# Performance work log

Hardware: AMD Instinct MI355X
Metric: run time of the kernel (lower is better)

## Reference

```python
import jax, jax.numpy as jnp
import numpy as np

B, T, D = 4, 2048, 1024
H = 16
HD = D // H  # 64


def setup_inputs() -> dict:
    key = jax.random.key(0)
    ks = jax.random.split(key, 5)
    scale = 0.02
    x = jax.random.normal(ks[0], (B, T, D), dtype=jnp.float32)
    W_qkv = jax.random.normal(ks[1], (D, 3 * D), dtype=jnp.float32) * scale
    b_qkv = jnp.zeros((3 * D,), dtype=jnp.float32)
    W_proj = jax.random.normal(ks[2], (D, D), dtype=jnp.float32) * scale
    b_proj = jnp.zeros((D,), dtype=jnp.float32)
    return {"x": x, "W_qkv": W_qkv, "b_qkv": b_qkv, "W_proj": W_proj, "b_proj": b_proj}


def reference(x, W_qkv, b_qkv, W_proj, b_proj):
    b, t, c = x.shape
    qkv = x @ W_qkv + b_qkv  # [b, t, 3c]
    q, k, v = jnp.split(qkv, 3, axis=-1)
    # [b, h, t, hd]
    q = q.reshape(b, t, H, HD).transpose(0, 2, 1, 3)
    k = k.reshape(b, t, H, HD).transpose(0, 2, 1, 3)
    v = v.reshape(b, t, H, HD).transpose(0, 2, 1, 3)
    att = jnp.einsum('bhqd,bhkd->bhqk', q, k) / jnp.sqrt(jnp.float32(HD))
    causal = jnp.tril(jnp.ones((t, t), dtype=bool))
    att = jnp.where(causal[None, None], att, jnp.float32(-jnp.inf))
    att = jax.nn.softmax(att, axis=-1)
    y = jnp.einsum('bhqk,bhkd->bhqd', att, v)
    y = y.transpose(0, 2, 1, 3).reshape(b, t, c)
    return y @ W_proj + b_proj
```

## Files before the change

kernel.cpp:

```cpp
#include <hip/hip_runtime.h>
#include <hip/hip_bf16.h>
#include <cmath>
#include <cstdint>

#define B_ 4
#define T_ 2048
#define D_ 1024
#define H_ 16
#define HD_ 64
#define M_ (B_*T_)
#define NQKV_ 3072

#define SCALE_Q 0.18033688011112042f

typedef float f32x4 __attribute__((ext_vector_type(4)));
typedef float f32x16 __attribute__((ext_vector_type(16)));
typedef __bf16 bf16x8 __attribute__((ext_vector_type(8)));
typedef __bf16 bf16x4 __attribute__((ext_vector_type(4)));

#define MFMA16(a, b, c) __builtin_amdgcn_mfma_f32_16x16x32_bf16((a), (b), (c), 0, 0, 0)
#define MFMA32(a, b, c) __builtin_amdgcn_mfma_f32_32x32x16_bf16((a), (b), (c), 0, 0, 0)

#if defined(__has_builtin)
#if __has_builtin(__builtin_amdgcn_global_load_lds)
#define HAVE_GLDS 1
#endif
#if __has_builtin(__builtin_amdgcn_permlane32_swap)
#define HAVE_PLSWAP 1
#endif
#endif

#ifdef HAVE_GLDS
#define GLDS16(g, l) __builtin_amdgcn_global_load_lds( \
    (const __attribute__((address_space(1))) void*)(g), \
    (__attribute__((address_space(3))) void*)(l), 16, 0, 0)
#endif

__device__ inline float hexp2(float x) {
  float r; asm("v_exp_f32 %0, %1" : "=v"(r) : "v"(x)); return r;
}

__device__ inline uint32_t pack2bf(float a, float b) {
  union { __bf16 h[2]; uint32_t u; } x;
  x.h[0] = (__bf16)a; x.h[1] = (__bf16)b;
  return x.u;
}

__global__ __launch_bounds__(256) void k_cvt_bf16(const float4* __restrict__ in,
                                                  bf16x4* __restrict__ out, int n4) {
  int i = blockIdx.x * 256 + threadIdx.x;
  if (i >= n4) return;
  float4 v = in[i];
  bf16x4 o;
  o[0] = (__bf16)v.x; o[1] = (__bf16)v.y; o[2] = (__bf16)v.z; o[3] = (__bf16)v.w;
  out[i] = o;
}

__global__ __launch_bounds__(256) void k_transpose_cvt(const float* __restrict__ in,
                                                       __bf16* __restrict__ out,
                                                       int R, int C) {
  __shared__ float tile[64][65];
  int r0 = blockIdx.y * 64, c0 = blockIdx.x * 64;
#pragma unroll
  for (int i = 0; i < 16; ++i) {
    int e = threadIdx.x + i * 256;
    int lr = e >> 6, lc = e & 63;
    tile[lr][lc] = in[(size_t)(r0 + lr) * C + c0 + lc];
  }
  __syncthreads();
#pragma unroll
  for (int i = 0; i < 16; ++i) {
    int e = threadIdx.x + i * 256;
    int lc = e >> 6, lr = e & 63;
    out[(size_t)(c0 + lc) * R + r0 + lr] = (__bf16)tile[lr][lc];
  }
}

__global__ __launch_bounds__(256) void k_gemm_qkv(const __bf16* __restrict__ A,
                                                  const __bf16* __restrict__ Bt,
                                                  const float* __restrict__ bias,
                                                  __bf16* __restrict__ Qb,
                                                  __bf16* __restrict__ Kb,
                                                  __bf16* __restrict__ Vt) {
  __shared__ __bf16 lA[128 * 64];
  __shared__ __bf16 lB[192 * 64];
  const int tid = threadIdx.x;
  const int lane = tid & 63, w = tid >> 6;
  const int wr = w >> 1, wc = w & 1;
  const int r15 = lane & 15, rg = lane >> 4;
  const int mb = blockIdx.y, nb = blockIdx.x;
  const int K = D_;
  const int nt = K >> 6;

  const f32x4 zero = {0.f, 0.f, 0.f, 0.f};
  f32x4 acc[4][6];
#pragma unroll
  for (int m = 0; m < 4; ++m)
#pragma unroll
    for (int n = 0; n < 6; ++n) acc[m][n] = zero;

  const __bf16* Ab = A + (size_t)(mb * 128) * K;
  const __bf16* Bb = Bt + (size_t)(nb * 192) * K;

  for (int t = 0; t < nt; ++t) {
    __syncthreads();
#pragma unroll
    for (int i = 0; i < 4; ++i) {
      const int c = tid + i * 256;
      const int rA = c >> 3, g = (c & 7) ^ (rA & 7);
#ifdef HAVE_GLDS
      GLDS16(Ab + (size_t)rA * K + t * 64 + g * 8, &lA[c * 8]);
#else
      bf16x8 v = *(const bf16x8*)(Ab + (size_t)rA * K + t * 64 + g * 8);
      *(bf16x8*)(&lA[c * 8]) = v;
#endif
    }
#pragma unroll
    for (int i = 0; i < 6; ++i) {
      const int c = tid + i * 256;
      const int rB = c >> 3, g = (c & 7) ^ (rB & 7);
#ifdef HAVE_GLDS
      GLDS16(Bb + (size_t)rB * K + t * 64 + g * 8, &lB[c * 8]);
#else
      bf16x8 v = *(const bf16x8*)(Bb + (size_t)rB * K + t * 64 + g * 8);
      *(bf16x8*)(&lB[c * 8]) = v;
#endif
    }
    __syncthreads();
#pragma unroll
    for (int ksub = 0; ksub < 2; ++ksub) {
      const int cc = (ksub * 4 + rg) ^ (r15 & 7);
      bf16x8 af[4];
#pragma unroll
      for (int m = 0; m < 4; ++m) {
        const int row = wr * 64 + m * 16 + r15;
        af[m] = *(const bf16x8*)(&lA[(row * 8 + cc) * 8]);
      }
#pragma unroll
      for (int n = 0; n < 6; ++n) {
        const int row = wc * 96 + n * 16 + r15;
        bf16x8 bfr = *(const bf16x8*)(&lB[(row * 8 + cc) * 8]);
#pragma unroll
        for (int m = 0; m < 4; ++m)
          acc[m][n] = MFMA16(af[m], bfr, acc[m][n]);
      }
    }
  }

  const int row0 = mb * 128 + wr * 64;
  const int col0 = nb * 192 + wc * 96;
#pragma unroll
  for (int m = 0; m < 4; ++m) {
#pragma unroll
    for (int n = 0; n < 6; ++n) {
      const int c = col0 + n * 16 + r15;
      const int r0 = row0 + m * 16 + rg * 4;
      const int which = c >> 10, cc = c & 1023;
      const int b = r0 >> 11, t0 = r0 & 2047;
      float v[4];
#pragma unroll
      for (int j = 0; j < 4; ++j) v[j] = acc[m][n][j] + bias[c];
      if (which == 0) {
        int hh = cc >> 6, hd = cc & 63;
#pragma unroll
        for (int j = 0; j < 4; ++j)
          Qb[((size_t)(b * H_ + hh) * T_ + t0 + j) * HD_ + hd] = (__bf16)(v[j] * SCALE_Q);
      } else if (which == 1) {
        int hh = cc >> 6, hd = cc & 63;
#pragma unroll
        for (int j = 0; j < 4; ++j)
          Kb[((size_t)(b * H_ + hh) * T_ + t0 + j) * HD_ + hd] = (__bf16)v[j];
      } else {
        int hh = cc >> 6, hd = cc & 63;
        bf16x4 pk;
#pragma unroll
        for (int j = 0; j < 4; ++j) pk[j] = (__bf16)v[j];
        *(bf16x4*)(Vt + ((size_t)(b * H_ + hh) * HD_ + hd) * T_ + t0) = pk;
      }
    }
  }
}

__global__ __launch_bounds__(256) void k_gemm_proj(const __bf16* __restrict__ A,
                                                   const __bf16* __restrict__ Bt,
                                                   const float* __restrict__ bias,
                                                   float* __restrict__ Cf,
                                                   int K, int N) {
  __shared__ __bf16 lA[128 * 64];
  __shared__ __bf16 lB[128 * 64];
  const int tid = threadIdx.x;
  const int lane = tid & 63, w = tid >> 6;
  const int wr = w >> 1, wc = w & 1;
  const int r15 = lane & 15, rg = lane >> 4;
  const int mb = blockIdx.y, nb = blockIdx.x;
  const int nt = K >> 6;

  const f32x4 zero = {0.f, 0.f, 0.f, 0.f};
  f32x4 acc[4][4];
#pragma unroll
  for (int m = 0; m < 4; ++m)
#pragma unroll
    for (int n = 0; n < 4; ++n) acc[m][n] = zero;

  const __bf16* Ab = A + (size_t)(mb * 128) * K;
  const __bf16* Bb = Bt + (size_t)(nb * 128) * K;

  for (int t = 0; t < nt; ++t) {
    __syncthreads();
#pragma unroll
    for (int i = 0; i < 4; ++i) {
      const int c = tid + i * 256;
      const int rA = c >> 3, g = (c & 7) ^ (rA & 7);
#ifdef HAVE_GLDS
      GLDS16(Ab + (size_t)rA * K + t * 64 + g * 8, &lA[c * 8]);
#else
      bf16x8 v = *(const bf16x8*)(Ab + (size_t)rA * K + t * 64 + g * 8);
      *(bf16x8*)(&lA[c * 8]) = v;
#endif
    }
#pragma unroll
    for (int i = 0; i < 4; ++i) {
      const int c = tid + i * 256;
      const int rB = c >> 3, g = (c & 7) ^ (rB & 7);
#ifdef HAVE_GLDS
      GLDS16(Bb + (size_t)rB * K + t * 64 + g * 8, &lB[c * 8]);
#else
      bf16x8 v = *(const bf16x8*)(Bb + (size_t)rB * K + t * 64 + g * 8);
      *(bf16x8*)(&lB[c * 8]) = v;
#endif
    }
    __syncthreads();
#pragma unroll
    for (int ksub = 0; ksub < 2; ++ksub) {
      bf16x8 af[4], bfr[4];
#pragma unroll
      for (int m = 0; m < 4; ++m) {
        const int row = wr * 64 + m * 16 + r15;
        const int cc = (ksub * 4 + rg) ^ (r15 & 7);
        af[m] = *(const bf16x8*)(&lA[(row * 8 + cc) * 8]);
      }
#pragma unroll
      for (int n = 0; n < 4; ++n) {
        const int row = wc * 64 + n * 16 + r15;
        const int cc = (ksub * 4 + rg) ^ (r15 & 7);
        bfr[n] = *(const bf16x8*)(&lB[(row * 8 + cc) * 8]);
      }
#pragma unroll
      for (int m = 0; m < 4; ++m)
#pragma unroll
        for (int n = 0; n < 4; ++n)
          acc[m][n] = MFMA16(af[m], bfr[n], acc[m][n]);
    }
  }

  const int row0 = mb * 128 + wr * 64;
  const int col0 = nb * 128 + wc * 64;
#pragma unroll
  for (int m = 0; m < 4; ++m)
#pragma unroll
    for (int n = 0; n < 4; ++n)
#pragma unroll
      for (int j = 0; j < 4; ++j) {
        int r = row0 + m * 16 + rg * 4 + j;
        int c = col0 + n * 16 + r15;
        Cf[(size_t)r * N + c] = acc[m][n][j] + bias[c];
      }
}

__global__ __launch_bounds__(256) void k_attn(const __bf16* __restrict__ Qb,
                                              const __bf16* __restrict__ Kb,
                                              const __bf16* __restrict__ Vt,
                                              __bf16* __restrict__ Obuf) {
  __shared__ __bf16 lK[2][64 * 64];
  __shared__ __bf16 lV[2][64 * 64];
  const int tid = threadIdx.x;
  const int lane = tid & 63, w = tid >> 6;
  const int l31 = lane & 31, hi = lane >> 5;
  const int bh = blockIdx.x;
  const int b = bh >> 4, h = bh & 15;
  const __bf16* Qh = Qb + (size_t)bh * T_ * HD_;
  const __bf16* Kh = Kb + (size_t)bh * T_ * HD_;
  const __bf16* Vh = Vt + (size_t)bh * HD_ * T_;

  const int sRow0 = tid >> 3, sSw0 = (((tid) & 7) ^ (sRow0 & 7)) * 8;
  const int c1s = tid + 256;
  const int sRow1 = c1s >> 3, sSw1 = ((c1s & 7) ^ (sRow1 & 7)) * 8;

  auto STAGE = [&](int bufi, int kv0) {
#ifdef HAVE_GLDS
    GLDS16(Kh + (size_t)(kv0 + sRow0) * HD_ + sSw0, &lK[bufi][tid * 8]);
    GLDS16(Kh + (size_t)(kv0 + sRow1) * HD_ + sSw1, &lK[bufi][(tid + 256) * 8]);
    GLDS16(Vh + (size_t)sRow0 * T_ + kv0 + sSw0, &lV[bufi][tid * 8]);
    GLDS16(Vh + (size_t)sRow1 * T_ + kv0 + sSw1, &lV[bufi][(tid + 256) * 8]);
#else
    bf16x8 k0 = *(const bf16x8*)(Kh + (size_t)(kv0 + sRow0) * HD_ + sSw0);
    bf16x8 k1 = *(const bf16x8*)(Kh + (size_t)(kv0 + sRow1) * HD_ + sSw1);
    bf16x8 v0 = *(const bf16x8*)(Vh + (size_t)sRow0 * T_ + kv0 + sSw0);
    bf16x8 v1 = *(const bf16x8*)(Vh + (size_t)sRow1 * T_ + kv0 + sSw1);
    *(bf16x8*)(&lK[bufi][tid * 8]) = k0;
    *(bf16x8*)(&lK[bufi][(tid + 256) * 8]) = k1;
    *(bf16x8*)(&lV[bufi][tid * 8]) = v0;
    *(bf16x8*)(&lV[bufi][(tid + 256) * 8]) = v1;
#endif
  };

  int buf = 0;
  STAGE(0, 0);

  auto process_half = [&](int s, int nst, bool hasNext) {
    const int q0w = s * 128 + w * 32;
    bf16x8 qf[4];
#pragma unroll
    for (int ks = 0; ks < 4; ++ks)
      qf[ks] = *(const bf16x8*)(Qh + (size_t)(q0w + l31) * HD_ + ks * 16 + hi * 8);

    f32x16 o0, o1;
#pragma unroll
    for (int i = 0; i < 16; ++i) { o0[i] = 0.f; o1[i] = 0.f; }
    float lpart = 0.f;

    for (int i = 0; i < nst; ++i) {
      const int kv0 = i * 64;
      if (i + 1 < nst) STAGE(buf ^ 1, (i + 1) * 64);
      else if (hasNext) STAGE(buf ^ 1, 0);

      if (kv0 <= q0w + 31) {
        const bool masked = (kv0 + 63) > q0w;
        bf16x8 kf[2][4];
#pragma unroll
        for (int seg = 0; seg < 2; ++seg)
#pragma unroll
          for (int ks = 0; ks < 4; ++ks)
            kf[seg][ks] = *(const bf16x8*)(&lK[buf][(seg * 32 + l31) * 64 +
                                                   (((ks * 2 + hi) ^ (l31 & 7)) * 8)]);
        f32x16 s0, s1;
#pragma unroll
        for (int r = 0; r < 16; ++r) { s0[r] = 0.f; s1[r] = 0.f; }
        __builtin_amdgcn_s_setprio(1);
#pragma unroll
        for (int ks = 0; ks < 4; ++ks) s0 = MFMA32(kf[0][ks], qf[ks], s0);
#pragma unroll
        for (int ks = 0; ks < 4; ++ks) s1 = MFMA32(kf[1][ks], qf[ks], s1);
        __builtin_amdgcn_s_setprio(0);

        if (masked) {
#pragma unroll
          for (int r = 0; r < 16; ++r) {
            int rr = (r & 3) + 8 * (r >> 2) + 4 * hi;
            if (kv0 + rr > q0w + l31) s0[r] = -INFINITY;
            if (kv0 + 32 + rr > q0w + l31) s1[r] = -INFINITY;
          }
        }
        float rs = 0.f;
#pragma unroll
        for (int r = 0; r < 16; ++r) {
          s0[r] = hexp2(s0[r]); s1[r] = hexp2(s1[r]);
          rs += s0[r] + s1[r];
        }
        lpart += rs;

        bf16x8 vf[2][4];
#pragma unroll
        for (int dh = 0; dh < 2; ++dh)
#pragma unroll
          for (int ks = 0; ks < 4; ++ks)
            vf[dh][ks] = *(const bf16x8*)(&lV[buf][(dh * 32 + l31) * 64 +
                                                   (((ks * 2 + hi) ^ (l31 & 7)) * 8)]);

#pragma unroll
        for (int ks = 0; ks < 4; ++ks) {
          const f32x16& sv = (ks < 2) ? s0 : s1;
          const int off = (ks & 1) * 8;
          uint32_t w0 = pack2bf(sv[off + 0], sv[off + 1]);
          uint32_t w1 = pack2bf(sv[off + 2], sv[off + 3]);
          uint32_t w2 = pack2bf(sv[off + 4], sv[off + 5]);
          uint32_t w3 = pack2bf(sv[off + 6], sv[off + 7]);
          union { uint32_t u[4]; bf16x8 v; } pa;
#ifdef HAVE_PLSWAP
          auto rA = __builtin_amdgcn_permlane32_swap((int)w0, (int)w2, false, false);
          auto rB = __builtin_amdgcn_permlane32_swap((int)w1, (int)w3, false, false);
          pa.u[0] = (uint32_t)rA[0];
          pa.u[1] = (uint32_t)rB[0];
          pa.u[2] = (uint32_t)rA[1];
          pa.u[3] = (uint32_t)rB[1];
#else
          uint32_t sx = hi ? w0 : w2;
          uint32_t sy = hi ? w1 : w3;
          uint32_t px = (uint32_t)__shfl_xor((int)sx, 32, 64);
          uint32_t py = (uint32_t)__shfl_xor((int)sy, 32, 64);
          pa.u[0] = hi ? px : w0;
          pa.u[1] = hi ? py : w1;
          pa.u[2] = hi ? w2 : px;
          pa.u[3] = hi ? w3 : py;
#endif
          __builtin_amdgcn_s_setprio(1);
          o0 = MFMA32(pa.v, vf[0][ks], o0);
          o1 = MFMA32(pa.v, vf[1][ks], o1);
          __builtin_amdgcn_s_setprio(0);
        }
      }
      __syncthreads();
      buf ^= 1;
    }

    float lrun = lpart + __shfl_xor(lpart, 32, 64);
#pragma unroll
    for (int r = 0; r < 16; ++r) {
      int rr = (r & 3) + 8 * (r >> 2) + 4 * hi;
      float inv = 1.0f / __shfl(lrun, rr, 64);
      int row = q0w + rr;
      __bf16* op = Obuf + (size_t)(b * T_ + row) * D_ + h * HD_ + l31;
      op[0]  = (__bf16)(o0[r] * inv);
      op[32] = (__bf16)(o1[r] * inv);
    }
  };

  const int sA = 15 - blockIdx.y;
  const int sB = blockIdx.y;
  __syncthreads();
  process_half(sA, 2 * sA + 2, true);
  process_half(sB, 2 * sB + 2, false);
}

extern "C" void kernel_launch(void* const* d_in, const int* in_sizes, int n_in,
                              void* d_out, int out_size, void* d_ws, size_t ws_size,
                              hipStream_t stream) {
  const float* x      = (const float*)d_in[0];
  const float* W_qkv  = (const float*)d_in[1];
  const float* b_qkv  = (const float*)d_in[2];
  const float* W_proj = (const float*)d_in[3];
  const float* b_proj = (const float*)d_in[4];
  float* out = (float*)d_out;

  char* ws = (char*)d_ws;
  size_t o = 0;
  __bf16* xb     = (__bf16*)(ws + o); o += (size_t)M_ * D_ * 2;
  __bf16* wqkvt  = (__bf16*)(ws + o); o += (size_t)NQKV_ * D_ * 2;
  __bf16* wprojt = (__bf16*)(ws + o); o += (size_t)D_ * D_ * 2;
  __bf16* Qb     = (__bf16*)(ws + o); o += (size_t)M_ * D_ * 2;
  __bf16* Kb     = (__bf16*)(ws + o); o += (size_t)M_ * D_ * 2;
  __bf16* Vt     = (__bf16*)(ws + o); o += (size_t)M_ * D_ * 2;
  __bf16* Obuf   = (__bf16*)(ws + o); o += (size_t)M_ * D_ * 2;
  (void)ws_size; (void)in_sizes; (void)n_in; (void)out_size;

  k_cvt_bf16<<<(M_ * D_ / 4 + 255) / 256, 256, 0, stream>>>((const float4*)x, (bf16x4*)xb, M_ * D_ / 4);
  k_transpose_cvt<<<dim3(NQKV_ / 64, D_ / 64), 256, 0, stream>>>(W_qkv, wqkvt, D_, NQKV_);
  k_transpose_cvt<<<dim3(D_ / 64, D_ / 64), 256, 0, stream>>>(W_proj, wprojt, D_, D_);
  k_gemm_qkv<<<dim3(NQKV_ / 192, M_ / 128), 256, 0, stream>>>(xb, wqkvt, b_qkv, Qb, Kb, Vt);
  k_attn<<<dim3(B_ * H_, 8), 256, 0, stream>>>(Qb, Kb, Vt, Obuf);
  k_gemm_proj<<<dim3(D_ / 128, M_ / 128), 256, 0, stream>>>(Obuf, wprojt, b_proj, out, D_, D_);
}
```

Baseline: 185.1 us.

## Double-buffer LDS tiles in QKV and projection GEMMs with K-step of 32

Both GEMM kernels now use two LDS buffers with a K tile of 32 instead of one buffer with a K tile of 64. The next tile's global-to-LDS loads are issued before computing on the current buffer, which also drops one barrier per iteration. The aim is to overlap memory latency with MFMA work. In exchange there are twice as many loop iterations, and the swizzle pattern changes to fit 4-chunk rows.

```diff
diff --git a/kernel.cpp b/kernel.cpp
--- a/kernel.cpp
+++ b/kernel.cpp
@@ -82,15 +82,15 @@
                                                   __bf16* __restrict__ Qb,
                                                   __bf16* __restrict__ Kb,
                                                   __bf16* __restrict__ Vt) {
-  __shared__ __bf16 lA[128 * 64];
-  __shared__ __bf16 lB[192 * 64];
+  __shared__ __bf16 lA[2][128 * 32];
+  __shared__ __bf16 lB[2][192 * 32];
   const int tid = threadIdx.x;
   const int lane = tid & 63, w = tid >> 6;
   const int wr = w >> 1, wc = w & 1;
   const int r15 = lane & 15, rg = lane >> 4;
   const int mb = blockIdx.y, nb = blockIdx.x;
   const int K = D_;
-  const int nt = K >> 6;
+  const int nt = K >> 5;
 
   const f32x4 zero = {0.f, 0.f, 0.f, 0.f};
   f32x4 acc[4][6];
@@ -102,49 +102,55 @@
   const __bf16* Ab = A + (size_t)(mb * 128) * K;
   const __bf16* Bb = Bt + (size_t)(nb * 192) * K;
 
+  auto STAGE = [&](int bufi, int t) {
+#pragma unroll
+    for (int i = 0; i < 2; ++i) {
+      const int c = tid + i * 256;
+      const int r = c >> 2, g = (c & 3) ^ ((r >> 1) & 3);
+#ifdef HAVE_GLDS
+      GLDS16(Ab + (size_t)r * K + t * 32 + g * 8, &lA[bufi][c * 8]);
+#else
+      bf16x8 v = *(const bf16x8*)(Ab + (size_t)r * K + t * 32 + g * 8);
+      *(bf16x8*)(&lA[bufi][c * 8]) = v;
+#endif
+    }
+#pragma unroll
+    for (int i = 0; i < 3; ++i) {
+      const int c = tid + i * 256;
+      const int r = c >> 2, g = (c & 3) ^ ((r >> 1) & 3);
+#ifdef HAVE_GLDS
+      GLDS16(Bb + (size_t)r * K + t * 32 + g * 8, &lB[bufi][c * 8]);
+#else
+      bf16x8 v = *(const bf16x8*)(Bb + (size_t)r * K + t * 32 + g * 8);
+      *(bf16x8*)(&lB[bufi][c * 8]) = v;
+#endif
+    }
+  };
+
+  int buf = 0;
+  STAGE(0, 0);
+  __syncthreads();
+
   for (int t = 0; t < nt; ++t) {
+    if (t + 1 < nt) STAGE(buf ^ 1, t + 1);
+    bf16x8 af[4];
+#pragma unroll
+    for (int m = 0; m < 4; ++m) {
+      const int row = wr * 64 + m * 16 + r15;
+      const int cc = rg ^ ((row >> 1) & 3);
+      af[m] = *(const bf16x8*)(&lA[buf][(row * 4 + cc) * 8]);
+    }
+#pragma unroll
+    for (int n = 0; n < 6; ++n) {
+      const int row = wc * 96 + n * 16 + r15;
+      const int cc = rg ^ ((row >> 1) & 3);
+      bf16x8 bfr = *(const bf16x8*)(&lB[buf][(row * 4 + cc) * 8]);
+#pragma unroll
+      for (int m = 0; m < 4; ++m)
+        acc[m][n] = MFMA16(af[m], bfr, acc[m][n]);
+    }
     __syncthreads();
-#pragma unroll
-    for (int i = 0; i < 4; ++i) {
-      const int c = tid + i * 256;
-      const int rA = c >> 3, g = (c & 7) ^ (rA & 7);
-#ifdef HAVE_GLDS
-      GLDS16(Ab + (size_t)rA * K + t * 64 + g * 8, &lA[c * 8]);
-#else
-      bf16x8 v = *(const bf16x8*)(Ab + (size_t)rA * K + t * 64 + g * 8);
-      *(bf16x8*)(&lA[c * 8]) = v;
-#endif
-    }
-#pragma unroll
-    for (int i = 0; i < 6; ++i) {
-      const int c = tid + i * 256;
-      const int rB = c >> 3, g = (c & 7) ^ (rB & 7);
-#ifdef HAVE_GLDS
-      GLDS16(Bb + (size_t)rB * K + t * 64 + g * 8, &lB[c * 8]);
-#else
-      bf16x8 v = *(const bf16x8*)(Bb + (size_t)rB * K + t * 64 + g * 8);
-      *(bf16x8*)(&lB[c * 8]) = v;
-#endif
-    }
-    __syncthreads();
-#pragma unroll
-    for (int ksub = 0; ksub < 2; ++ksub) {
-      const int cc = (ksub * 4 + rg) ^ (r15 & 7);
-      bf16x8 af[4];
-#pragma unroll
-      for (int m = 0; m < 4; ++m) {
-        const int row = wr * 64 + m * 16 + r15;
-        af[m] = *(const bf16x8*)(&lA[(row * 8 + cc) * 8]);
-      }
-#pragma unroll
-      for (int n = 0; n < 6; ++n) {
-        const int row = wc * 96 + n * 16 + r15;
-        bf16x8 bfr = *(const bf16x8*)(&lB[(row * 8 + cc) * 8]);
-#pragma unroll
-        for (int m = 0; m < 4; ++m)
-          acc[m][n] = MFMA16(af[m], bfr, acc[m][n]);
-      }
-    }
+    buf ^= 1;
   }
 
   const int row0 = mb * 128 + wr * 64;
@@ -186,14 +192,14 @@
                                                    const float* __restrict__ bias,
                                                    float* __restrict__ Cf,
                                                    int K, int N) {
-  __shared__ __bf16 lA[128 * 64];
-  __shared__ __bf16 lB[128 * 64];
+  __shared__ __bf16 lA[2][128 * 32];
+  __shared__ __bf16 lB[2][128 * 32];
   const int tid = threadIdx.x;
   const int lane = tid & 63, w = tid >> 6;
   const int wr = w >> 1, wc = w & 1;
   const int r15 = lane & 15, rg = lane >> 4;
   const int mb = blockIdx.y, nb = blockIdx.x;
-  const int nt = K >> 6;
+  const int nt = K >> 5;
 
   const f32x4 zero = {0.f, 0.f, 0.f, 0.f};
   f32x4 acc[4][4];
@@ -205,52 +211,49 @@
   const __bf16* Ab = A + (size_t)(mb * 128) * K;
   const __bf16* Bb = Bt + (size_t)(nb * 128) * K;
 
+  auto STAGE = [&](int bufi, int t) {
+#pragma unroll
+    for (int i = 0; i < 2; ++i) {
+      const int c = tid + i * 256;
+      const int r = c >> 2, g = (c & 3) ^ ((r >> 1) & 3);
+#ifdef HAVE_GLDS
+      GLDS16(Ab + (size_t)r * K + t * 32 + g * 8, &lA[bufi][c * 8]);
+      GLDS16(Bb + (size_t)r * K + t * 32 + g * 8, &lB[bufi][c * 8]);
+#else
+      bf16x8 va = *(const bf16x8*)(Ab + (size_t)r * K + t * 32 + g * 8);
+      bf16x8 vb = *(const bf16x8*)(Bb + (size_t)r * K + t * 32 + g * 8);
+      *(bf16x8*)(&lA[bufi][c * 8]) = va;
+      *(bf16x8*)(&lB[bufi][c * 8]) = vb;
+#endif
+    }
+  };
+
+  int buf = 0;
+  STAGE(0, 0);
+  __syncthreads();
+
   for (int t = 0; t < nt; ++t) {
+    if (t + 1 < nt) STAGE(buf ^ 1, t + 1);
+    bf16x8 af[4], bfr[4];
+#pragma unroll
+    for (int m = 0; m < 4; ++m) {
+      const int row = wr * 64 + m * 16 + r15;
+      const int cc = rg ^ ((row >> 1) & 3);
+      af[m] = *(const bf16x8*)(&lA[buf][(row * 4 + cc) * 8]);
+    }
+#pragma unroll
+    for (int n = 0; n < 4; ++n) {
+      const int row = wc * 64 + n * 16 + r15;
+      const int cc = rg ^ ((row >> 1) & 3);
+      bfr[n] = *(const bf16x8*)(&lB[buf][(row * 4 + cc) * 8]);
+    }
+#pragma unroll
+    for (int m = 0; m < 4; ++m)
+#pragma unroll
+      for (int n = 0; n < 4; ++n)
+        acc[m][n] = MFMA16(af[m], bfr[n], acc[m][n]);
     __syncthreads();
-#pragma unroll
-    for (int i = 0; i < 4; ++i) {
-      const int c = tid + i * 256;
-      const int rA = c >> 3, g = (c & 7) ^ (rA & 7);
-#ifdef HAVE_GLDS
-      GLDS16(Ab + (size_t)rA * K + t * 64 + g * 8, &lA[c * 8]);
-#else
-      bf16x8 v = *(const bf16x8*)(Ab + (size_t)rA * K + t * 64 + g * 8);
-      *(bf16x8*)(&lA[c * 8]) = v;
-#endif
-    }
-#pragma unroll
-    for (int i = 0; i < 4; ++i) {
-      const int c = tid + i * 256;
-      const int rB = c >> 3, g = (c & 7) ^ (rB & 7);
-#ifdef HAVE_GLDS
-      GLDS16(Bb + (size_t)rB * K + t * 64 + g * 8, &lB[c * 8]);
-#else
-      bf16x8 v = *(const bf16x8*)(Bb + (size_t)rB * K + t * 64 + g * 8);
-      *(bf16x8*)(&lB[c * 8]) = v;
-#endif
-    }
-    __syncthreads();
-#pragma unroll
-    for (int ksub = 0; ksub < 2; ++ksub) {
-      bf16x8 af[4], bfr[4];
-#pragma unroll
-      for (int m = 0; m < 4; ++m) {
-        const int row = wr * 64 + m * 16 + r15;
-        const int cc = (ksub * 4 + rg) ^ (r15 & 7);
-        af[m] = *(const bf16x8*)(&lA[(row * 8 + cc) * 8]);
-      }
-#pragma unroll
-      for (int n = 0; n < 4; ++n) {
-        const int row = wc * 64 + n * 16 + r15;
-        const int cc = (ksub * 4 + rg) ^ (r15 & 7);
-        bfr[n] = *(const bf16x8*)(&lB[(row * 8 + cc) * 8]);
-      }
-#pragma unroll
-      for (int m = 0; m < 4; ++m)
-#pragma unroll
-        for (int n = 0; n < 4; ++n)
-          acc[m][n] = MFMA16(af[m], bfr[n], acc[m][n]);
-    }
+    buf ^= 1;
   }
 
   const int row0 = mb * 128 + wr * 64;
```

After: 201.9 us. 1.09x slower.
